# Optimization experiments

Measured on AMD Instinct MI355X. Metric: run time of the kernel, lower is better.

Reference implementation:

```python
import jax, jax.numpy as jnp
import numpy as np


def setup_inputs() -> dict:
    key = jax.random.key(0)
    k1, k2 = jax.random.split(key)
    B, S, H, E = 8, 4096, 16, 64
    s = int(S ** 0.5)  # 64
    v = jax.random.normal(k1, (B, S, H, E), dtype=jnp.float32)
    w = jax.random.normal(k2, (1, H, 2 * s - 1), dtype=jnp.float32)  # 'full' bias base
    o_ = jnp.ones((s,), dtype=jnp.float32)
    return {"v": v, "w": w, "o_": o_}


def reference(v, w, o_):
    # FFTBias2d forward, bias_base_type='full', has_specials=False.
    B, S, H, E = v.shape
    s = int(S ** 0.5)  # grid side; S == s*s

    # z = w[..., shape_-seq_len : shape_+seq_len-1] with seq_len==shape_ -> whole w (len 2s-1)
    z = w[..., s - s : s + s - 1]          # (1, H, 2s-1)
    z_fft = jnp.fft.rfft(z)                # (1, H, s)

    # [B,S,H,E] -> [B,E,H,S] -> [B,E,H,s,s] -> [B,E,s,H,s]
    v_ = jnp.transpose(v, (0, 3, 2, 1)).reshape(B, E, H, s, s)
    v_ = jnp.transpose(v_, (0, 1, 3, 2, 4))

    # row-sum path: sum over first grid axis -> [B,E,H,s]
    v_s = v_.sum(-3)
    v_m = jnp.pad(v_s, ((0, 0), (0, 0), (0, 0), (s - 1, 0)))  # len 2s-1
    v_m_fft = jnp.fft.rfft(v_m)

    # col-sum path: [B,E,s2,H,s1] summed over s2 -> [B,E,H,s]
    u_s = jnp.transpose(v_, (0, 1, 4, 3, 2)).sum(-3)
    u_m = jnp.pad(u_s, ((0, 0), (0, 0), (0, 0), (s - 1, 0)))
    u_m_fft = jnp.fft.rfft(u_m)

    zf = jnp.expand_dims(z_fft, axis=1)    # (1, 1, H, s) broadcasts vs (B, E, H, s)
    RxV_m = jnp.fft.irfft(v_m_fft * zf)[..., :s]  # (B, E, H, s)
    RxU_m = jnp.fft.irfft(u_m_fft * zf)[..., :s]

    # outer sum over the two grid axes -> (B, E, H, s, s) -> (B, S, H, E)
    pbv = RxV_m[..., None, :] + RxU_m[..., :, None]
    pbv = pbv.reshape(B, E, H, S)
    pbv = jnp.transpose(pbv, (0, 3, 2, 1))

    # normalizer path
    o_pad = jnp.pad(o_, (s - 1, 0))        # len 2s-1
    o_fft = jnp.fft.rfft(o_pad)            # (s,)
    z_pb = jnp.fft.irfft(o_fft * z_fft)[..., :s] * s  # (1, H, s)
    z_pb = z_pb[..., None, :] + z_pb[..., :, None]    # (1, H, s, s)
    z_pb = z_pb.reshape(-1, H, S)
    z_pb = jnp.transpose(z_pb, (0, 2, 1))  # (1, S, H)
    return pbv, z_pb
```

## Files before the change

### kernel.cpp

```cpp
#include <hip/hip_runtime.h>
#include <stdint.h>

#define OUT2_OFF 33554432ull

typedef float v4f __attribute__((ext_vector_type(4)));

__global__ __launch_bounds__(256) void fused1_kernel(
        const float* __restrict__ v,
        const float* __restrict__ wgt,
        float* __restrict__ us,
        float* __restrict__ vs_part,
        float* __restrict__ G) {
    const int bid = blockIdx.x;
    const int tid = threadIdx.x;

    if (bid < 512) {
        const int ig = bid & 3, bh = bid >> 2;
        const int b = bh >> 4, h = bh & 15;
        const int w = tid >> 6, lane = tid & 63;
        const int rs = lane & 15;
        const int q  = 4 * w + (lane >> 4);

        const v4f* v4 = (const v4f*)v;
        const size_t base4 = (size_t)b * 1048576 + (size_t)h * 16 + q;

        v4f vsacc[4];
#pragma unroll
        for (int a = 0; a < 4; ++a) vsacc[a] = (v4f)0.f;
        v4f cur[4], nxt[4];

        {
            const int t0 = (ig * 16) * 64;
#pragma unroll
            for (int jh = 0; jh < 4; ++jh)
                cur[jh] = __builtin_nontemporal_load(
                    v4 + base4 + (size_t)(t0 + jh * 16 + rs) * 256);
        }
        for (int il = 0; il < 16; ++il) {
            const int i = ig * 16 + il;
            if (il < 15) {
#pragma unroll
                for (int jh = 0; jh < 4; ++jh)
                    nxt[jh] = __builtin_nontemporal_load(
                        v4 + base4 + (size_t)((i + 1) * 64 + jh * 16 + rs) * 256);
            }
            v4f p = (v4f)0.f;
#pragma unroll
            for (int jh = 0; jh < 4; ++jh) {
                p += cur[jh];
                vsacc[jh] += cur[jh];
            }
#pragma unroll
            for (int mask = 1; mask <= 8; mask <<= 1) {
                p.x += __shfl_xor(p.x, mask);
                p.y += __shfl_xor(p.y, mask);
                p.z += __shfl_xor(p.z, mask);
                p.w += __shfl_xor(p.w, mask);
            }
            if (rs == 0)
                *(v4f*)(us + ((size_t)bh * 64 + i) * 64 + q * 4) = p;
#pragma unroll
            for (int jh = 0; jh < 4; ++jh) cur[jh] = nxt[jh];
        }
#pragma unroll
        for (int jh = 0; jh < 4; ++jh) {
            const int j = jh * 16 + rs;
            *(v4f*)(vs_part + (((size_t)ig * 128 + bh) * 64 + j) * 64 + q * 4) =
                vsacc[jh];
        }
    } else {
        const int pb = bid - 512;
        const int h = pb >> 4, tq = pb & 15;
        __shared__ float zl[127];
        __shared__ float c127t[127], s127t[127];
        __shared__ float c126t[126], s126t[126];
        __shared__ float ZA[64], ZB[64];
        const float w127 = 6.28318530717958647692f / 127.0f;
        const float w126 = 6.28318530717958647692f / 126.0f;
        if (tid < 127) {
            zl[tid] = wgt[h * 127 + tid];
            float sv, cv; __sincosf((float)tid * w127, &sv, &cv);
            c127t[tid] = cv; s127t[tid] = sv;
        } else if (tid >= 128 && tid < 254) {
            const int m = tid - 128;
            float sv, cv; __sincosf((float)m * w126, &sv, &cv);
            c126t[m] = cv; s126t[m] = sv;
        }
        __syncthreads();
        if (tid < 64) {
            const int k = tid;
            float a = 0.f, bq = 0.f;
            int r = 0;
            for (int m = 0; m < 127; ++m) {
                a  += zl[m] * c127t[r];
                bq -= zl[m] * s127t[r];
                r += k; if (r >= 127) r -= 127;
            }
            ZA[k] = a; ZB[k] = bq;
        }
        __syncthreads();
        const int t = tq * 4 + (tid >> 6);
        const int j = tid & 63;
        const int jj = 63 + j;
        float acc = ZA[0];
        int rb = t, ra = jj;
        for (int k = 1; k <= 62; ++k) {
            const float cA = c126t[rb], sA = s126t[rb];
            const float cB = c127t[ra], sB = s127t[ra];
            const float cAB = cA * cB + sA * sB;
            const float sAB = sA * cB - cA * sB;
            acc += 2.f * (ZA[k] * cAB - ZB[k] * sAB);
            rb += t;  if (rb >= 126) rb -= 126;
            ra += jj; if (ra >= 127) ra -= 127;
        }
        {
            const int rn = (63 * jj) % 127;
            const float term = ZA[63] * c127t[rn] + ZB[63] * s127t[rn];
            acc += (t & 1) ? -term : term;
        }
        G[((size_t)h * 64 + t) * 64 + j] = acc * (1.0f / 126.0f);
    }
}

__global__ __launch_bounds__(256) void convemit_kernel(
        const float* __restrict__ G,
        const float* __restrict__ us,
        const float* __restrict__ vs_part,
        const float* __restrict__ ovec,
        float* __restrict__ out) {
    const int bid = blockIdx.x;
    const int tid = threadIdx.x;

    __shared__ float GlT[64 * 68];
    __shared__ float usl[4096];
    __shared__ float vsl[4096];
    __shared__ float rxv_l[64 * 68];
    __shared__ float rxu_l[16 * 68];
    __shared__ float zpb[1024];
    __shared__ float ol[64];

    if (bid < 512) {
        const int bh = bid >> 2, tq = bid & 3;
        const int b = bh >> 4, h = bh & 15;

        for (int k = 0; k < 16; ++k) {
            const int idx = k * 256 + tid;
            usl[idx] = us[(size_t)bh * 4096 + idx];
            float a = 0.f;
#pragma unroll
            for (int ig = 0; ig < 4; ++ig)
                a += vs_part[((size_t)ig * 128 + bh) * 4096 + idx];
            vsl[idx] = a;
            GlT[(idx & 63) * 68 + (idx >> 6)] = G[(size_t)h * 4096 + idx];
        }
        __syncthreads();

        const int tb = tid >> 4;
        const int q  = tid & 15;
        const int i_row = tq * 16 + tb;
        const v4f* us4 = (const v4f*)usl;
        const v4f* vs4 = (const v4f*)vsl;

        v4f accV[4];
#pragma unroll
        for (int r = 0; r < 4; ++r) accV[r] = (v4f)0.f;
        v4f accU = (v4f)0.f;
#pragma unroll 8
        for (int j = 0; j < 64; ++j) {
            const v4f gv = *(const v4f*)&GlT[j * 68 + tb * 4];
            const float gu = GlT[j * 68 + i_row];
            const v4f vv = vs4[j * 16 + q];
            const v4f uu = us4[j * 16 + q];
            accV[0] += gv.x * vv;
            accV[1] += gv.y * vv;
            accV[2] += gv.z * vv;
            accV[3] += gv.w * vv;
            accU += gu * uu;
        }
#pragma unroll
        for (int r = 0; r < 4; ++r)
            *(v4f*)&rxv_l[(tb * 4 + r) * 68 + q * 4] = accV[r];
        *(v4f*)&rxu_l[tb * 68 + q * 4] = accU;
        __syncthreads();

        const int w = tid >> 6, lane = tid & 63;
        float rv[16];
#pragma unroll
        for (int jj = 0; jj < 16; ++jj)
            rv[jj] = rxv_l[(jj * 4 + w) * 68 + lane];
        const size_t obase = (((size_t)b * 4096 + tq * 1024) * 16 + h) * 64 + lane;
        for (int il = 0; il < 16; ++il) {
            const float ru = rxu_l[il * 68 + lane];
#pragma unroll
            for (int jj = 0; jj < 16; ++jj) {
                const int j = jj * 4 + w;
                __builtin_nontemporal_store(rv[jj] + ru,
                    out + obase + (size_t)(il * 64 + j) * 1024);
            }
        }
    } else {
        const int bz = bid - 512;
        if (tid < 64) ol[tid] = ovec[tid];
        __syncthreads();
#pragma unroll
        for (int r = 0; r < 4; ++r) {
            const int idx = tid + 256 * r;
            const int h = idx >> 6, n = idx & 63;
            float acc = 0.f;
            for (int j = 0; j < 64; ++j)
                acc += ol[j] * G[(size_t)h * 4096 + n * 64 + j];
            zpb[idx] = acc * 64.f;
        }
        __syncthreads();
#pragma unroll
        for (int r = 0; r < 4; ++r) {
            const int k = tid + 256 * r;
            const int hh = k & 15, c = k >> 4;
            out[OUT2_OFF + ((size_t)(bz * 64 + c)) * 16 + hh] =
                zpb[hh * 64 + c] + zpb[hh * 64 + bz];
        }
    }
}

extern "C" void kernel_launch(void* const* d_in, const int* in_sizes, int n_in,
                              void* d_out, int out_size, void* d_ws, size_t ws_size,
                              hipStream_t stream) {
    const float* v    = (const float*)d_in[0];
    const float* wgt  = (const float*)d_in[1];
    const float* ovec = (const float*)d_in[2];

    float* G       = (float*)d_ws;
    float* us      = G + 65536;
    float* vs_part = us + 524288;
    float* out     = (float*)d_out;

    hipLaunchKernelGGL(fused1_kernel,   dim3(512 + 256), dim3(256), 0, stream,
                       v, wgt, us, vs_part, G);
    hipLaunchKernelGGL(convemit_kernel, dim3(512 + 64),  dim3(256), 0, stream,
                       G, us, vs_part, ovec, out);
}
```

Baseline: 251.5 us.

## Batch shuffle reductions, vectorize loads and output stores with float4

The column-sum reduction in the first kernel now buffers 8 rows at a time and reduces them with a transpose-style butterfly, cutting shuffle count from 16 per row to about 2 per row, with a bit-reversed row index for the final store. The second kernel loads us, vs_part and G as float4, and emits the main output as float4 nontemporal stores instead of scalar stores. The normalizer dot product is vectorized too. In exchange, register pressure rises from the fully unrolled loop and the 8-entry accumulator array.

Measured after the change: 248.0 us. Within noise of the previous version (-1.4%).

```diff
diff --git a/kernel.cpp b/kernel.cpp
--- a/kernel.cpp
+++ b/kernel.cpp
@@ -4,6 +4,33 @@
 #define OUT2_OFF 33554432ull
 
 typedef float v4f __attribute__((ext_vector_type(4)));
+
+__device__ __forceinline__ v4f shflx4(v4f s, int m) {
+    v4f r;
+    r.x = __shfl_xor(s.x, m);
+    r.y = __shfl_xor(s.y, m);
+    r.z = __shfl_xor(s.z, m);
+    r.w = __shfl_xor(s.w, m);
+    return r;
+}
+
+__device__ __forceinline__ v4f reduce8(v4f* A, int rs) {
+#pragma unroll
+    for (int k = 0; k < 4; ++k) {
+        v4f s = (rs & 2) ? A[k] : A[k + 4];
+        v4f r = shflx4(s, 2);
+        A[k] = ((rs & 2) ? A[k + 4] : A[k]) + r;
+    }
+#pragma unroll
+    for (int k = 0; k < 2; ++k) {
+        v4f s = (rs & 4) ? A[k] : A[k + 2];
+        v4f r = shflx4(s, 4);
+        A[k] = ((rs & 4) ? A[k + 2] : A[k]) + r;
+    }
+    v4f s = (rs & 8) ? A[0] : A[1];
+    v4f r = shflx4(s, 8);
+    return ((rs & 8) ? A[1] : A[0]) + r;
+}
 
 __global__ __launch_bounds__(256) void fused1_kernel(
         const float* __restrict__ v,
@@ -27,15 +54,14 @@
         v4f vsacc[4];
 #pragma unroll
         for (int a = 0; a < 4; ++a) vsacc[a] = (v4f)0.f;
-        v4f cur[4], nxt[4];
-
-        {
-            const int t0 = (ig * 16) * 64;
-#pragma unroll
-            for (int jh = 0; jh < 4; ++jh)
-                cur[jh] = __builtin_nontemporal_load(
-                    v4 + base4 + (size_t)(t0 + jh * 16 + rs) * 256);
-        }
+        v4f A[8], cur[4], nxt[4], R0;
+
+#pragma unroll
+        for (int jh = 0; jh < 4; ++jh)
+            cur[jh] = __builtin_nontemporal_load(
+                v4 + base4 + (size_t)(ig * 1024 + jh * 16 + rs) * 256);
+
+#pragma unroll
         for (int il = 0; il < 16; ++il) {
             const int i = ig * 16 + il;
             if (il < 15) {
@@ -44,23 +70,22 @@
                     nxt[jh] = __builtin_nontemporal_load(
                         v4 + base4 + (size_t)((i + 1) * 64 + jh * 16 + rs) * 256);
             }
-            v4f p = (v4f)0.f;
-#pragma unroll
-            for (int jh = 0; jh < 4; ++jh) {
-                p += cur[jh];
-                vsacc[jh] += cur[jh];
-            }
-#pragma unroll
-            for (int mask = 1; mask <= 8; mask <<= 1) {
-                p.x += __shfl_xor(p.x, mask);
-                p.y += __shfl_xor(p.y, mask);
-                p.z += __shfl_xor(p.z, mask);
-                p.w += __shfl_xor(p.w, mask);
-            }
-            if (rs == 0)
-                *(v4f*)(us + ((size_t)bh * 64 + i) * 64 + q * 4) = p;
+            v4f p = (cur[0] + cur[1]) + (cur[2] + cur[3]);
+#pragma unroll
+            for (int jh = 0; jh < 4; ++jh) vsacc[jh] += cur[jh];
+            A[il & 7] = p;
+            if (il == 7) R0 = reduce8(A, rs);
 #pragma unroll
             for (int jh = 0; jh < 4; ++jh) cur[jh] = nxt[jh];
+        }
+        v4f R1 = reduce8(A, rs);
+        {
+            v4f s = (rs & 1) ? R0 : R1;
+            v4f r = shflx4(s, 1);
+            v4f res = ((rs & 1) ? R1 : R0) + r;
+            const int ir = ((rs & 1) << 3) | (((rs >> 1) & 1) << 2) |
+                           (((rs >> 2) & 1) << 1) | ((rs >> 3) & 1);
+            *(v4f*)(us + ((size_t)bh * 64 + ig * 16 + ir) * 64 + q * 4) = res;
         }
 #pragma unroll
         for (int jh = 0; jh < 4; ++jh) {
@@ -131,71 +156,87 @@
     const int bid = blockIdx.x;
     const int tid = threadIdx.x;
 
-    __shared__ float GlT[64 * 68];
-    __shared__ float usl[4096];
-    __shared__ float vsl[4096];
-    __shared__ float rxv_l[64 * 68];
-    __shared__ float rxu_l[16 * 68];
-    __shared__ float zpb[1024];
-    __shared__ float ol[64];
+    __shared__ __align__(16) float GlT[64 * 68];
+    __shared__ __align__(16) float usl[4096];
+    __shared__ __align__(16) float vsl[4096];
+    __shared__ __align__(16) float rxv_l[64 * 68];
+    __shared__ __align__(16) float rxu_l[16 * 68];
+    __shared__ __align__(16) float zpb[1024];
+    __shared__ __align__(16) float ol[64];
 
     if (bid < 512) {
         const int bh = bid >> 2, tq = bid & 3;
         const int b = bh >> 4, h = bh & 15;
 
-        for (int k = 0; k < 16; ++k) {
-            const int idx = k * 256 + tid;
-            usl[idx] = us[(size_t)bh * 4096 + idx];
-            float a = 0.f;
-#pragma unroll
-            for (int ig = 0; ig < 4; ++ig)
-                a += vs_part[((size_t)ig * 128 + bh) * 4096 + idx];
-            vsl[idx] = a;
-            GlT[(idx & 63) * 68 + (idx >> 6)] = G[(size_t)h * 4096 + idx];
-        }
-        __syncthreads();
-
-        const int tb = tid >> 4;
-        const int q  = tid & 15;
-        const int i_row = tq * 16 + tb;
-        const v4f* us4 = (const v4f*)usl;
-        const v4f* vs4 = (const v4f*)vsl;
-
-        v4f accV[4];
-#pragma unroll
-        for (int r = 0; r < 4; ++r) accV[r] = (v4f)0.f;
-        v4f accU = (v4f)0.f;
+        const v4f* usg = (const v4f*)(us + (size_t)bh * 4096);
+        const v4f* vp0 = (const v4f*)(vs_part + (size_t)bh * 4096);
+        const v4f* vp1 = (const v4f*)(vs_part + (size_t)(128 + bh) * 4096);
+        const v4f* vp2 = (const v4f*)(vs_part + (size_t)(256 + bh) * 4096);
+        const v4f* vp3 = (const v4f*)(vs_part + (size_t)(384 + bh) * 4096);
+        const v4f* Gg  = (const v4f*)(G + (size_t)h * 4096);
+
+#pragma unroll
+        for (int k = 0; k < 4; ++k) {
+            const int vi = k * 256 + tid;
+            const int fi = vi * 4;
+            v4f uu = usg[vi];
+            *(v4f*)&usl[fi] = uu;
+            v4f a = (vp0[vi] + vp1[vi]) + (vp2[vi] + vp3[vi]);
+            *(v4f*)&vsl[fi] = a;
+            v4f g = Gg[vi];
+            const int t = fi >> 6, j0 = fi & 63;
+            GlT[(j0 + 0) * 68 + t] = g.x;
+            GlT[(j0 + 1) * 68 + t] = g.y;
+            GlT[(j0 + 2) * 68 + t] = g.z;
+            GlT[(j0 + 3) * 68 + t] = g.w;
+        }
+        __syncthreads();
+
+        {
+            const int tb = tid >> 4;
+            const int q  = tid & 15;
+            const int i_row = tq * 16 + tb;
+            const v4f* us4 = (const v4f*)usl;
+            const v4f* vs4 = (const v4f*)vsl;
+
+            v4f accV[4];
+#pragma unroll
+            for (int r = 0; r < 4; ++r) accV[r] = (v4f)0.f;
+            v4f accU = (v4f)0.f;
 #pragma unroll 8
-        for (int j = 0; j < 64; ++j) {
-            const v4f gv = *(const v4f*)&GlT[j * 68 + tb * 4];
-            const float gu = GlT[j * 68 + i_row];
-            const v4f vv = vs4[j * 16 + q];
-            const v4f uu = us4[j * 16 + q];
-            accV[0] += gv.x * vv;
-            accV[1] += gv.y * vv;
-            accV[2] += gv.z * vv;
-            accV[3] += gv.w * vv;
-            accU += gu * uu;
-        }
-#pragma unroll
-        for (int r = 0; r < 4; ++r)
-            *(v4f*)&rxv_l[(tb * 4 + r) * 68 + q * 4] = accV[r];
-        *(v4f*)&rxu_l[tb * 68 + q * 4] = accU;
+            for (int j = 0; j < 64; ++j) {
+                const v4f gv = *(const v4f*)&GlT[j * 68 + tb * 4];
+                const float gu = GlT[j * 68 + i_row];
+                const v4f vv = vs4[j * 16 + q];
+                const v4f uu = us4[j * 16 + q];
+                accV[0] += gv.x * vv;
+                accV[1] += gv.y * vv;
+                accV[2] += gv.z * vv;
+                accV[3] += gv.w * vv;
+                accU += gu * uu;
+            }
+#pragma unroll
+            for (int r = 0; r < 4; ++r)
+                *(v4f*)&rxv_l[(tb * 4 + r) * 68 + q * 4] = accV[r];
+            *(v4f*)&rxu_l[tb * 68 + q * 4] = accU;
+        }
         __syncthreads();
 
         const int w = tid >> 6, lane = tid & 63;
-        float rv[16];
-#pragma unroll
-        for (int jj = 0; jj < 16; ++jj)
-            rv[jj] = rxv_l[(jj * 4 + w) * 68 + lane];
-        const size_t obase = (((size_t)b * 4096 + tq * 1024) * 16 + h) * 64 + lane;
+        const int jsub = lane >> 4, qq = lane & 15;
+        v4f rv4[4];
+#pragma unroll
+        for (int jj = 0; jj < 4; ++jj)
+            rv4[jj] = *(const v4f*)&rxv_l[(jj * 16 + w * 4 + jsub) * 68 + qq * 4];
+        const size_t obase =
+            (((size_t)b * 4096 + tq * 1024) * 16 + h) * 64 + qq * 4;
         for (int il = 0; il < 16; ++il) {
-            const float ru = rxu_l[il * 68 + lane];
-#pragma unroll
-            for (int jj = 0; jj < 16; ++jj) {
-                const int j = jj * 4 + w;
-                __builtin_nontemporal_store(rv[jj] + ru,
-                    out + obase + (size_t)(il * 64 + j) * 1024);
+            const v4f ru = *(const v4f*)&rxu_l[il * 68 + qq * 4];
+#pragma unroll
+            for (int jj = 0; jj < 4; ++jj) {
+                const int j = jj * 16 + w * 4 + jsub;
+                __builtin_nontemporal_store(rv4[jj] + ru,
+                    (v4f*)(out + obase + (size_t)(il * 64 + j) * 1024));
             }
         }
     } else {
@@ -206,10 +247,12 @@
         for (int r = 0; r < 4; ++r) {
             const int idx = tid + 256 * r;
             const int h = idx >> 6, n = idx & 63;
-            float acc = 0.f;
-            for (int j = 0; j < 64; ++j)
-                acc += ol[j] * G[(size_t)h * 4096 + n * 64 + j];
-            zpb[idx] = acc * 64.f;
+            const v4f* G4 = (const v4f*)(G + (size_t)h * 4096 + n * 64);
+            v4f acc4 = (v4f)0.f;
+#pragma unroll
+            for (int jv = 0; jv < 16; ++jv)
+                acc4 += (*(const v4f*)&ol[jv * 4]) * G4[jv];
+            zpb[idx] = (acc4.x + acc4.y + acc4.z + acc4.w) * 64.f;
         }
         __syncthreads();
 #pragma unroll
```
